# Performance work log

Measured on AMD Instinct MI355X. Metric: run time of the kernel, lower is better.

The kernel has to match this reference:

```python
import jax, jax.numpy as jnp
import numpy as np
from jax import lax

N, C_IN, C_OUT, H, W, K = 32, 512, 512, 56, 56, 7


def setup_inputs() -> dict:
    key = jax.random.key(0)
    ks = jax.random.split(key, 7)
    s_in = 1.0 / np.sqrt(C_IN)
    s_out = 1.0 / np.sqrt(C_OUT)
    return {
        "x": jax.random.normal(ks[0], (N, C_IN, H, W), dtype=jnp.float32),
        "k": K,
        "w_up": jax.random.normal(ks[1], (C_OUT, C_IN), dtype=jnp.float32) * s_in,
        "b_up": jax.random.normal(ks[2], (C_OUT,), dtype=jnp.float32) * s_in,
        "w_down": jax.random.normal(ks[3], (C_OUT, C_IN), dtype=jnp.float32) * s_in,
        "b_down": jax.random.normal(ks[4], (C_OUT,), dtype=jnp.float32) * s_in,
        "w_final": jax.random.normal(ks[5], (C_OUT, C_OUT), dtype=jnp.float32) * s_out,
        "b_final": jax.random.normal(ks[6], (C_OUT,), dtype=jnp.float32) * s_out,
    }


def _conv1x1(x, w, b):
    # x: [N, Cin, H, W], w: [Cout, Cin] -> [N, Cout, H, W]
    return jnp.einsum("nchw,oc->nohw", x, w) + b[None, :, None, None]


def reference(x, k, w_up, b_up, w_down, b_down, w_final, b_final):
    n, c_in, h, w = x.shape
    c_out = w_up.shape[0]
    pad = (k - 1) // 2

    up = _conv1x1(x, w_up, b_up)  # [N, Cout, H, W]

    # AdaptiveAvgPool2d(k): H, W divisible by k -> exact uniform pooling
    pooled = x.reshape(n, c_in, k, h // k, k, w // k).mean(axis=(3, 5))  # [N, Cin, k, k]
    down = _conv1x1(pooled, w_down, b_down)  # [N, Cout, k, k] dynamic depthwise kernels

    def dw_conv(u, ker):
        # u: [Cout, H, W], ker: [Cout, k, k]; depthwise (groups = Cout)
        return lax.conv_general_dilated(
            u[None],                    # [1, Cout, H, W]
            ker[:, None],               # [Cout, 1, k, k] (OIHW)
            window_strides=(1, 1),
            padding=[(pad, pad), (pad, pad)],
            feature_group_count=c_out,
            dimension_numbers=("NCHW", "OIHW", "NCHW"),
        )[0]

    out = jax.vmap(dw_conv)(up, down)  # [N, Cout, H, W]
    return _conv1x1(out, w_final, b_final)
```

## Files before the change

kernel.cpp:

```cpp
#include <hip/hip_runtime.h>
#include <hip/hip_bf16.h>

typedef unsigned short u16;
typedef _Float16 f16x8 __attribute__((ext_vector_type(8)));
typedef _Float16 f16x4 __attribute__((ext_vector_type(4)));
typedef _Float16 half2v __attribute__((ext_vector_type(2)));
typedef float f32x4 __attribute__((ext_vector_type(4)));
typedef unsigned short ushortx8 __attribute__((ext_vector_type(8)));
typedef unsigned short ushortx4 __attribute__((ext_vector_type(4)));

#define GPTR(p)  ((const __attribute__((address_space(1))) void*)(p))
#define LDSPTR(p) ((__attribute__((address_space(3))) void*)(p))

static __device__ __forceinline__ u16 f2h(float f) {
    _Float16 h = (_Float16)f;
    union { _Float16 h; u16 u; } v; v.h = h; return v.u;
}

__global__ __launch_bounds__(256) void cvtw_kernel(
    const float* __restrict__ wu, const float* __restrict__ wf,
    u16* __restrict__ wub, u16* __restrict__ wfb) {
    int i = blockIdx.x * 256 + threadIdx.x;
    wub[i] = f2h(wu[i]);
    wfb[i] = f2h(wf[i]);
}

__global__ __launch_bounds__(256) void transpose_kernel(
    const float* __restrict__ x, u16* __restrict__ xt) {
    __shared__ float tile[64][65];
    int bid = blockIdx.x;
    int jt = bid % 49;
    int r = bid / 49;
    int ct = r & 7, n = r >> 3;
    const float* src = x + ((size_t)(n * 512 + ct * 64)) * 3136 + jt * 64;
    for (int e = threadIdx.x; e < 4096; e += 256) {
        int i = e >> 6, jj = e & 63;
        tile[i][jj] = src[(size_t)i * 3136 + jj];
    }
    __syncthreads();
    u16* dst = xt + ((size_t)(n * 3136 + jt * 64)) * 512 + ct * 64;
    for (int e = threadIdx.x; e < 2048; e += 256) {
        int jj = e >> 5, i2 = (e & 31) * 2;
        unsigned int val = (unsigned)f2h(tile[i2][jj]) | ((unsigned)f2h(tile[i2 + 1][jj]) << 16);
        *(unsigned int*)(dst + (size_t)jj * 512 + i2) = val;
    }
}

__global__ __launch_bounds__(256) void poolh_kernel(
    const u16* __restrict__ xt, float* __restrict__ pooled) {
    int bid = blockIdx.x;
    int n = bid / 49, cell = bid - n * 49;
    int py = cell / 7, px = cell - py * 7;
    int t = threadIdx.x;
    float s0 = 0.f, s1 = 0.f;
    for (int r = 0; r < 8; ++r) {
        int h = py * 8 + r;
        const u16* base = xt + ((size_t)(n * 3136 + h * 56 + px * 8)) * 512 + 2 * t;
        #pragma unroll
        for (int cc = 0; cc < 8; ++cc) {
            half2v v = *(const half2v*)(base + (size_t)cc * 512);
            s0 += (float)v[0]; s1 += (float)v[1];
        }
    }
    float* pp = pooled + (size_t)n * 512 * 49 + py * 7 + px;
    pp[(size_t)(2 * t) * 49]     = s0 * (1.f / 64.f);
    pp[(size_t)(2 * t + 1) * 49] = s1 * (1.f / 64.f);
}

__global__ __launch_bounds__(256) void down_kernel(
    const float* __restrict__ pooled, const float* __restrict__ w_down,
    const float* __restrict__ b_down, float* __restrict__ down) {
    int bid = blockIdx.x;
    int n = bid >> 5, og = bid & 31;
    int wv = threadIdx.x >> 6, lane = threadIdx.x & 63;
    int o0 = og * 16 + wv * 4;
    const float* pp = pooled + (size_t)n * 512 * 49;
    const float* w0 = w_down + (size_t)o0 * 512;
    float a0 = 0, a1 = 0, a2 = 0, a3 = 0;
    int cell = lane < 49 ? lane : 48;
    #pragma unroll 4
    for (int c = 0; c < 512; ++c) {
        float p = pp[c * 49 + cell];
        a0 += p * w0[c];
        a1 += p * w0[512 + c];
        a2 += p * w0[1024 + c];
        a3 += p * w0[1536 + c];
    }
    if (lane < 49) {
        float* dd = down + ((size_t)n * 512 + o0) * 49 + lane;
        dd[0]   = a0 + b_down[o0];
        dd[49]  = a1 + b_down[o0 + 1];
        dd[98]  = a2 + b_down[o0 + 2];
        dd[147] = a3 + b_down[o0 + 3];
    }
}

template <int EPI>
__global__ __launch_bounds__(256) void gemm_kernel(
    const u16* __restrict__ A, const u16* __restrict__ Bt,
    const float* __restrict__ bias, void* __restrict__ Cout) {
    constexpr int K = 512;
    __shared__ u16 As[128 * 32];
    __shared__ u16 Bs[128 * 32];
    int tid = threadIdx.x, wv = tid >> 6, lane = tid & 63;
    int bid = blockIdx.x;
    int tm, tn;
    if (EPI == 0) { tm = (bid >> 5) * 8 + (bid & 7); tn = (bid >> 3) & 3; }
    else          { tn = (bid >> 5) * 8 + (bid & 7); tm = (bid >> 3) & 3; }
    size_t m0 = (size_t)tm * 128, n0 = (size_t)tn * 128;
    int lr = lane & 15, lk = (lane >> 4) * 8;
    int wr = wv >> 1, wc = wv & 1;

    int e0 = wv * 512 + lane * 8;
    int e1 = e0 + 2048;
    const u16* pa0 = A + (m0 + (size_t)(e0 >> 5)) * K + (e0 & 31);
    const u16* pa1 = A + (m0 + (size_t)(e1 >> 5)) * K + (e1 & 31);
    const u16* pb0 = Bt + (n0 + (size_t)(e0 >> 5)) * K + (e0 & 31);
    const u16* pb1 = Bt + (n0 + (size_t)(e1 >> 5)) * K + (e1 & 31);
    u16* sa0 = &As[wv * 512]; u16* sa1 = &As[wv * 512 + 2048];
    u16* sb0 = &Bs[wv * 512]; u16* sb1 = &Bs[wv * 512 + 2048];

    f32x4 acc[4][4] = {};

    for (int kt = 0; kt < K / 32; ++kt) {
        __builtin_amdgcn_global_load_lds(GPTR(pa0), LDSPTR(sa0), 16, 0, 0);
        __builtin_amdgcn_global_load_lds(GPTR(pa1), LDSPTR(sa1), 16, 0, 0);
        __builtin_amdgcn_global_load_lds(GPTR(pb0), LDSPTR(sb0), 16, 0, 0);
        __builtin_amdgcn_global_load_lds(GPTR(pb1), LDSPTR(sb1), 16, 0, 0);
        pa0 += 32; pa1 += 32; pb0 += 32; pb1 += 32;
        __syncthreads();
        f16x8 af[4], bfr[4];
        #pragma unroll
        for (int mi = 0; mi < 4; ++mi)
            af[mi] = *(const f16x8*)&As[(wr * 64 + mi * 16 + lr) * 32 + lk];
        #pragma unroll
        for (int ni = 0; ni < 4; ++ni)
            bfr[ni] = *(const f16x8*)&Bs[(wc * 64 + ni * 16 + lr) * 32 + lk];
        #pragma unroll
        for (int mi = 0; mi < 4; ++mi)
            #pragma unroll
            for (int ni = 0; ni < 4; ++ni)
                acc[mi][ni] = __builtin_amdgcn_mfma_f32_16x16x32_f16(af[mi], bfr[ni], acc[mi][ni], 0, 0, 0);
        __syncthreads();
    }

    if (EPI == 0) {
        u16* C = (u16*)Cout;
        #pragma unroll
        for (int ni = 0; ni < 4; ++ni) {
            size_t col = n0 + wc * 64 + ni * 16 + lr;
            float bv = bias[col];
            #pragma unroll
            for (int mi = 0; mi < 4; ++mi) {
                size_t rowb = m0 + wr * 64 + mi * 16 + (lane >> 4) * 4;
                ushortx4 pack;
                #pragma unroll
                for (int r = 0; r < 4; ++r)
                    pack[r] = f2h(acc[mi][ni][r] + bv);
                *(ushortx4*)&C[(rowb >> 3) * 4096 + col * 8 + (rowb & 7)] = pack;
            }
        }
    } else {
        float* C = (float*)Cout;
        #pragma unroll
        for (int ni = 0; ni < 4; ++ni) {
            int col = (int)(n0 + wc * 64 + ni * 16 + lr);
            int nimg = col / 3136;
            int jj = col - nimg * 3136;
            size_t obase = (size_t)nimg * 512 * 3136 + jj;
            #pragma unroll
            for (int mi = 0; mi < 4; ++mi) {
                int row = (int)(m0 + wr * 64 + mi * 16 + (lane >> 4) * 4);
                #pragma unroll
                for (int r = 0; r < 4; ++r)
                    C[obase + (size_t)(row + r) * 3136] = acc[mi][ni][r] + bias[row + r];
            }
        }
    }
}

__global__ __launch_bounds__(256) void dw_kernel(
    const u16* __restrict__ upb, const float* __restrict__ down,
    u16* __restrict__ dw) {
    __shared__ u16 tile[14 * 16 * 72];
    int bid = blockIdx.x;
    int n = bid / 224;
    int rem = bid - n * 224;
    int rt = rem >> 5;
    int cg = rem & 31;
    int tid = threadIdx.x;

    if (tid < 224)
        *(ushortx8*)&tile[tid * 72 + 56] = (ushortx8)0;

    for (int e = tid; e < 1568; e += 256) {
        int c = e & 15;
        int p = e >> 4;
        int hh = p / 7, jb = p - hh * 7;
        int h = rt * 8 + hh - 3;
        ushortx8 v = (ushortx8)0;
        if ((unsigned)h < 56u)
            v = *(const ushortx8*)(upb + ((size_t)(n * 392 + h * 7 + jb)) * 4096 + (cg * 16 + c) * 8);
        *(ushortx8*)&tile[(hh * 16 + c) * 72 + jb * 8] = v;
    }

    int c = tid & 15, u = tid >> 4;
    int row = u >> 1, wh = u & 1, w0 = wh * 28;
    const float* kp = down + ((size_t)n * 512 + cg * 16 + c) * 49;
    half2v kE[7][4], kO[7][4];
    #pragma unroll
    for (int ky = 0; ky < 7; ++ky) {
        float k0 = kp[ky*7+0], k1 = kp[ky*7+1], k2 = kp[ky*7+2], k3 = kp[ky*7+3];
        float k4 = kp[ky*7+4], k5 = kp[ky*7+5], k6 = kp[ky*7+6];
        kE[ky][0] = half2v{(_Float16)0.f, (_Float16)k0};
        kE[ky][1] = half2v{(_Float16)k1,  (_Float16)k2};
        kE[ky][2] = half2v{(_Float16)k3,  (_Float16)k4};
        kE[ky][3] = half2v{(_Float16)k5,  (_Float16)k6};
        kO[ky][0] = half2v{(_Float16)k0,  (_Float16)k1};
        kO[ky][1] = half2v{(_Float16)k2,  (_Float16)k3};
        kO[ky][2] = half2v{(_Float16)k4,  (_Float16)k5};
        kO[ky][3] = half2v{(_Float16)k6,  (_Float16)0.f};
    }
    __syncthreads();

    float acc[28];
    #pragma unroll
    for (int i = 0; i < 28; ++i) acc[i] = 0.f;

    #pragma unroll
    for (int ky = 0; ky < 7; ++ky) {
        const u16* rp = &tile[((row + ky) * 16 + c) * 72];
        half2v w2[18];
        #pragma unroll
        for (int t = 0; t < 9; ++t) {
            int p0 = ((w0 >> 1) - 2 + 2 * t) & 31;
            f16x4 q = *(const f16x4*)(rp + p0 * 2);
            w2[2*t]   = half2v{q[0], q[1]};
            w2[2*t+1] = half2v{q[2], q[3]};
        }
        #pragma unroll
        for (int m = 0; m < 14; ++m) {
            float ae = acc[2*m], ao = acc[2*m+1];
            ae = __builtin_amdgcn_fdot2(w2[m],   kE[ky][0], ae, false);
            ae = __builtin_amdgcn_fdot2(w2[m+1], kE[ky][1], ae, false);
            ae = __builtin_amdgcn_fdot2(w2[m+2], kE[ky][2], ae, false);
            ae = __builtin_amdgcn_fdot2(w2[m+3], kE[ky][3], ae, false);
            ao = __builtin_amdgcn_fdot2(w2[m+1], kO[ky][0], ao, false);
            ao = __builtin_amdgcn_fdot2(w2[m+2], kO[ky][1], ao, false);
            ao = __builtin_amdgcn_fdot2(w2[m+3], kO[ky][2], ao, false);
            ao = __builtin_amdgcn_fdot2(w2[m+4], kO[ky][3], ao, false);
            acc[2*m] = ae; acc[2*m+1] = ao;
        }
    }

    int h = rt * 8 + row;
    u16* op = dw + ((size_t)(n * 3136 + h * 56 + w0)) * 512 + cg * 16 + c;
    #pragma unroll
    for (int i = 0; i < 28; ++i)
        op[(size_t)i * 512] = f2h(acc[i]);
}

extern "C" void kernel_launch(void* const* d_in, const int* in_sizes, int n_in,
                              void* d_out, int out_size, void* d_ws, size_t ws_size,
                              hipStream_t stream) {
    const float* x       = (const float*)d_in[0];
    const float* w_up    = (const float*)d_in[2];
    const float* b_up    = (const float*)d_in[3];
    const float* w_down  = (const float*)d_in[4];
    const float* b_down  = (const float*)d_in[5];
    const float* w_final = (const float*)d_in[6];
    const float* b_final = (const float*)d_in[7];

    char* ws = (char*)d_ws;
    u16*   xt     = (u16*)  (ws + 0);
    u16*   upb    = (u16*)  (ws + 102760448);
    float* pooled = (float*)(ws + 205520896);
    float* down   = (float*)(ws + 208732160);
    u16*   wub    = (u16*)  (ws + 211943424);
    u16*   wfb    = (u16*)  (ws + 212467712);
    u16*   dwb    = xt;

    cvtw_kernel<<<1024, 256, 0, stream>>>(w_up, w_final, wub, wfb);
    transpose_kernel<<<12544, 256, 0, stream>>>(x, xt);
    poolh_kernel<<<1568, 256, 0, stream>>>(xt, pooled);
    down_kernel<<<1024, 256, 0, stream>>>(pooled, w_down, b_down, down);
    gemm_kernel<0><<<3136, 256, 0, stream>>>(xt, wub, b_up, upb);
    dw_kernel<<<7168, 256, 0, stream>>>(upb, down, dwb);
    gemm_kernel<1><<<3136, 256, 0, stream>>>(wfb, dwb, b_final, d_out);
}
```

Measured before the change: 410.6 us.

## Double-buffer GEMM LDS tiles and reorder depthwise block mapping

The GEMM main loop now uses two LDS buffers, prefetching the next K-slice via global_load_lds while MFMAs run on the current slice. This replaces two syncthreads per iteration with one waitcnt plus barrier, aiming to hide global load latency at the cost of doubled LDS (32KB per block), which may lower occupancy. The depthwise kernel's block index decomposition is also reordered so that consecutive blocks share a row tile across images and channel groups, changing L2 access locality.

```diff
diff --git a/kernel.cpp b/kernel.cpp
--- a/kernel.cpp
+++ b/kernel.cpp
@@ -100,8 +100,8 @@
     const u16* __restrict__ A, const u16* __restrict__ Bt,
     const float* __restrict__ bias, void* __restrict__ Cout) {
     constexpr int K = 512;
-    __shared__ u16 As[128 * 32];
-    __shared__ u16 Bs[128 * 32];
+    __shared__ u16 As[2][4096];
+    __shared__ u16 Bs[2][4096];
     int tid = threadIdx.x, wv = tid >> 6, lane = tid & 63;
     int bid = blockIdx.x;
     int tm, tn;
@@ -117,31 +117,44 @@
     const u16* pa1 = A + (m0 + (size_t)(e1 >> 5)) * K + (e1 & 31);
     const u16* pb0 = Bt + (n0 + (size_t)(e0 >> 5)) * K + (e0 & 31);
     const u16* pb1 = Bt + (n0 + (size_t)(e1 >> 5)) * K + (e1 & 31);
-    u16* sa0 = &As[wv * 512]; u16* sa1 = &As[wv * 512 + 2048];
-    u16* sb0 = &Bs[wv * 512]; u16* sb1 = &Bs[wv * 512 + 2048];
 
     f32x4 acc[4][4] = {};
 
+    {
+        __builtin_amdgcn_global_load_lds(GPTR(pa0), LDSPTR(&As[0][wv * 512]), 16, 0, 0);
+        __builtin_amdgcn_global_load_lds(GPTR(pa1), LDSPTR(&As[0][wv * 512 + 2048]), 16, 0, 0);
+        __builtin_amdgcn_global_load_lds(GPTR(pb0), LDSPTR(&Bs[0][wv * 512]), 16, 0, 0);
+        __builtin_amdgcn_global_load_lds(GPTR(pb1), LDSPTR(&Bs[0][wv * 512 + 2048]), 16, 0, 0);
+        pa0 += 32; pa1 += 32; pb0 += 32; pb1 += 32;
+    }
+    asm volatile("s_waitcnt vmcnt(0)" ::: "memory");
+    __builtin_amdgcn_s_barrier();
+
+    int cur = 0;
     for (int kt = 0; kt < K / 32; ++kt) {
-        __builtin_amdgcn_global_load_lds(GPTR(pa0), LDSPTR(sa0), 16, 0, 0);
-        __builtin_amdgcn_global_load_lds(GPTR(pa1), LDSPTR(sa1), 16, 0, 0);
-        __builtin_amdgcn_global_load_lds(GPTR(pb0), LDSPTR(sb0), 16, 0, 0);
-        __builtin_amdgcn_global_load_lds(GPTR(pb1), LDSPTR(sb1), 16, 0, 0);
-        pa0 += 32; pa1 += 32; pb0 += 32; pb1 += 32;
-        __syncthreads();
+        if (kt < K / 32 - 1) {
+            int nb = cur ^ 1;
+            __builtin_amdgcn_global_load_lds(GPTR(pa0), LDSPTR(&As[nb][wv * 512]), 16, 0, 0);
+            __builtin_amdgcn_global_load_lds(GPTR(pa1), LDSPTR(&As[nb][wv * 512 + 2048]), 16, 0, 0);
+            __builtin_amdgcn_global_load_lds(GPTR(pb0), LDSPTR(&Bs[nb][wv * 512]), 16, 0, 0);
+            __builtin_amdgcn_global_load_lds(GPTR(pb1), LDSPTR(&Bs[nb][wv * 512 + 2048]), 16, 0, 0);
+            pa0 += 32; pa1 += 32; pb0 += 32; pb1 += 32;
+        }
         f16x8 af[4], bfr[4];
         #pragma unroll
         for (int mi = 0; mi < 4; ++mi)
-            af[mi] = *(const f16x8*)&As[(wr * 64 + mi * 16 + lr) * 32 + lk];
+            af[mi] = *(const f16x8*)&As[cur][(wr * 64 + mi * 16 + lr) * 32 + lk];
         #pragma unroll
         for (int ni = 0; ni < 4; ++ni)
-            bfr[ni] = *(const f16x8*)&Bs[(wc * 64 + ni * 16 + lr) * 32 + lk];
+            bfr[ni] = *(const f16x8*)&Bs[cur][(wc * 64 + ni * 16 + lr) * 32 + lk];
         #pragma unroll
         for (int mi = 0; mi < 4; ++mi)
             #pragma unroll
             for (int ni = 0; ni < 4; ++ni)
                 acc[mi][ni] = __builtin_amdgcn_mfma_f32_16x16x32_f16(af[mi], bfr[ni], acc[mi][ni], 0, 0, 0);
-        __syncthreads();
+        asm volatile("s_waitcnt vmcnt(0)" ::: "memory");
+        __builtin_amdgcn_s_barrier();
+        cur ^= 1;
     }
 
     if (EPI == 0) {
@@ -184,10 +197,10 @@
     u16* __restrict__ dw) {
     __shared__ u16 tile[14 * 16 * 72];
     int bid = blockIdx.x;
-    int n = bid / 224;
-    int rem = bid - n * 224;
-    int rt = rem >> 5;
-    int cg = rem & 31;
+    int rt = bid >> 10;
+    int pair = bid & 1023;
+    int n = pair >> 5;
+    int cg = pair & 31;
     int tid = threadIdx.x;
 
     if (tid < 224)
```

Result: slower. 426.6 us (+3.9%).

## Triple-buffer GEMM LDS tiles with async prefetch two stages ahead

Applied to the files above, without the earlier changes.

Replaces the single-buffered load-sync-compute loop in the fp16 MFMA GEMM with a three-stage LDS ring. Global-to-LDS loads for tile kt+2 are issued before computing tile kt, and explicit vmcnt waits let earlier tiles finish while later ones are still in flight. The goal is to hide global memory latency behind MFMA work. In exchange it triples the LDS footprint, which may lower occupancy, and it depends on hand-counted vmcnt values being correct.

```diff
diff --git a/kernel.cpp b/kernel.cpp
--- a/kernel.cpp
+++ b/kernel.cpp
@@ -95,13 +95,21 @@
     }
 }
 
+#define STAGE(buf) do { \
+    __builtin_amdgcn_global_load_lds(GPTR(pa0), LDSPTR(&As[buf][wv * 512]), 16, 0, 0); \
+    __builtin_amdgcn_global_load_lds(GPTR(pa1), LDSPTR(&As[buf][wv * 512 + 2048]), 16, 0, 0); \
+    __builtin_amdgcn_global_load_lds(GPTR(pb0), LDSPTR(&Bs[buf][wv * 512]), 16, 0, 0); \
+    __builtin_amdgcn_global_load_lds(GPTR(pb1), LDSPTR(&Bs[buf][wv * 512 + 2048]), 16, 0, 0); \
+    pa0 += 32; pa1 += 32; pb0 += 32; pb1 += 32; } while (0)
+
 template <int EPI>
 __global__ __launch_bounds__(256) void gemm_kernel(
     const u16* __restrict__ A, const u16* __restrict__ Bt,
     const float* __restrict__ bias, void* __restrict__ Cout) {
     constexpr int K = 512;
-    __shared__ u16 As[128 * 32];
-    __shared__ u16 Bs[128 * 32];
+    constexpr int NT = K / 32;
+    __shared__ u16 As[3][4096];
+    __shared__ u16 Bs[3][4096];
     int tid = threadIdx.x, wv = tid >> 6, lane = tid & 63;
     int bid = blockIdx.x;
     int tm, tn;
@@ -117,31 +125,40 @@
     const u16* pa1 = A + (m0 + (size_t)(e1 >> 5)) * K + (e1 & 31);
     const u16* pb0 = Bt + (n0 + (size_t)(e0 >> 5)) * K + (e0 & 31);
     const u16* pb1 = Bt + (n0 + (size_t)(e1 >> 5)) * K + (e1 & 31);
-    u16* sa0 = &As[wv * 512]; u16* sa1 = &As[wv * 512 + 2048];
-    u16* sb0 = &Bs[wv * 512]; u16* sb1 = &Bs[wv * 512 + 2048];
 
     f32x4 acc[4][4] = {};
 
-    for (int kt = 0; kt < K / 32; ++kt) {
-        __builtin_amdgcn_global_load_lds(GPTR(pa0), LDSPTR(sa0), 16, 0, 0);
-        __builtin_amdgcn_global_load_lds(GPTR(pa1), LDSPTR(sa1), 16, 0, 0);
-        __builtin_amdgcn_global_load_lds(GPTR(pb0), LDSPTR(sb0), 16, 0, 0);
-        __builtin_amdgcn_global_load_lds(GPTR(pb1), LDSPTR(sb1), 16, 0, 0);
-        pa0 += 32; pa1 += 32; pb0 += 32; pb1 += 32;
-        __syncthreads();
+    STAGE(0);
+    STAGE(1);
+
+    int cur = 0, stg = 2;
+    for (int kt = 0; kt < NT; ++kt) {
+        if (kt + 2 < NT) {
+            STAGE(stg);
+            asm volatile("s_waitcnt vmcnt(8)" ::: "memory");
+        } else if (kt + 1 < NT) {
+            asm volatile("s_waitcnt vmcnt(4)" ::: "memory");
+        } else {
+            asm volatile("s_waitcnt vmcnt(0)" ::: "memory");
+        }
+        __builtin_amdgcn_s_barrier();
+
         f16x8 af[4], bfr[4];
         #pragma unroll
         for (int mi = 0; mi < 4; ++mi)
-            af[mi] = *(const f16x8*)&As[(wr * 64 + mi * 16 + lr) * 32 + lk];
+            af[mi] = *(const f16x8*)&As[cur][(wr * 64 + mi * 16 + lr) * 32 + lk];
         #pragma unroll
         for (int ni = 0; ni < 4; ++ni)
-            bfr[ni] = *(const f16x8*)&Bs[(wc * 64 + ni * 16 + lr) * 32 + lk];
+            bfr[ni] = *(const f16x8*)&Bs[cur][(wc * 64 + ni * 16 + lr) * 32 + lk];
         #pragma unroll
         for (int mi = 0; mi < 4; ++mi)
             #pragma unroll
             for (int ni = 0; ni < 4; ++ni)
                 acc[mi][ni] = __builtin_amdgcn_mfma_f32_16x16x32_f16(af[mi], bfr[ni], acc[mi][ni], 0, 0, 0);
-        __syncthreads();
+
+        __builtin_amdgcn_s_barrier();
+        cur = (cur == 2) ? 0 : cur + 1;
+        stg = (stg == 2) ? 0 : stg + 1;
     }
 
     if (EPI == 0) {
```

Measured after the change: 413.8 us. No clear change (+0.8%).

## Rewrite 1x1-conv GEMMs as 8-wave 128x256 tiles with multi-stage LDS pipeline

Applied to the files above, without the earlier changes.

Both GEMM launches now use a 512-thread kernel that computes 128x256 output tiles instead of 128x128. Operand tiles are prefetched into multi-buffered LDS (up to four stages) with global_load_lds, and the LDS layout uses an XOR swizzle. Split barriers and s_setprio interleave the prefetch issue with MFMA blocks. The aim is to hide global-load latency, avoid the two full __syncthreads per k-step, and cut LDS bank conflicts and per-tile operand traffic. In exchange it uses more LDS per block, which may limit occupancy, and depends on hand-tuned vmcnt waits being correct.

```diff
diff --git a/kernel.cpp b/kernel.cpp
--- a/kernel.cpp
+++ b/kernel.cpp
@@ -95,53 +95,88 @@
     }
 }
 
+#define STAGE_M(bufi, kt) do { \
+    __builtin_amdgcn_global_load_lds(GPTR(srcM + (size_t)(kt) * 32), LDSPTR(&Mb[bufi][wv * 512]), 16, 0, 0); \
+  } while (0)
+#define STAGE_N(bufi, kt) do { \
+    __builtin_amdgcn_global_load_lds(GPTR(srcN + (size_t)(kt) * 32), LDSPTR(&Nb[bufi][wv * 512]), 16, 0, 0); \
+    __builtin_amdgcn_global_load_lds(GPTR(srcN + 65536 + (size_t)(kt) * 32), LDSPTR(&Nb[bufi][4096 + wv * 512]), 16, 0, 0); \
+  } while (0)
+
 template <int EPI>
-__global__ __launch_bounds__(256) void gemm_kernel(
+__global__ __launch_bounds__(512, 4) void gemm8_kernel(
     const u16* __restrict__ A, const u16* __restrict__ Bt,
     const float* __restrict__ bias, void* __restrict__ Cout) {
-    constexpr int K = 512;
-    __shared__ u16 As[128 * 32];
-    __shared__ u16 Bs[128 * 32];
-    int tid = threadIdx.x, wv = tid >> 6, lane = tid & 63;
+    constexpr int NT = 16;
+    constexpr int DM = EPI ? 2 : 4;
+    constexpr int DN = EPI ? 4 : 2;
+    constexpr int SLoads = EPI ? 1 : 2;
+    __shared__ u16 Mb[DM][4096];
+    __shared__ u16 Nb[DN][8192];
+
+    int tid = threadIdx.x;
+    int wv = tid >> 6, l = tid & 63;
+    int lr = l & 15, lk = (l >> 4) * 8;
+    int wr = wv & 1, wc = wv >> 1;
     int bid = blockIdx.x;
     int tm, tn;
-    if (EPI == 0) { tm = (bid >> 5) * 8 + (bid & 7); tn = (bid >> 3) & 3; }
+    if (EPI == 0) { tm = (bid >> 4) * 8 + (bid & 7); tn = (bid >> 3) & 1; }
     else          { tn = (bid >> 5) * 8 + (bid & 7); tm = (bid >> 3) & 3; }
-    size_t m0 = (size_t)tm * 128, n0 = (size_t)tn * 128;
-    int lr = lane & 15, lk = (lane >> 4) * 8;
-    int wr = wv >> 1, wc = wv & 1;
-
-    int e0 = wv * 512 + lane * 8;
-    int e1 = e0 + 2048;
-    const u16* pa0 = A + (m0 + (size_t)(e0 >> 5)) * K + (e0 & 31);
-    const u16* pa1 = A + (m0 + (size_t)(e1 >> 5)) * K + (e1 & 31);
-    const u16* pb0 = Bt + (n0 + (size_t)(e0 >> 5)) * K + (e0 & 31);
-    const u16* pb1 = Bt + (n0 + (size_t)(e1 >> 5)) * K + (e1 & 31);
-    u16* sa0 = &As[wv * 512]; u16* sa1 = &As[wv * 512 + 2048];
-    u16* sb0 = &Bs[wv * 512]; u16* sb1 = &Bs[wv * 512 + 2048];
+    size_t m0 = (size_t)tm * 128, n0 = (size_t)tn * 256;
+
+    int r = tid >> 2;
+    int kx = ((tid & 3) * 8) ^ (((r >> 1) & 3) << 3);
+    const u16* srcM = A  + (m0 + (size_t)r) * 512 + kx;
+    const u16* srcN = Bt + (n0 + (size_t)r) * 512 + kx;
+    int aswz = ((lr >> 1) & 3) << 3;
+
+    if (EPI == 0) { STAGE_M(0, 0); STAGE_M(1, 1); STAGE_M(2, 2); STAGE_N(0, 0); STAGE_N(1, 1); }
+    else          { STAGE_N(0, 0); STAGE_N(1, 1); STAGE_N(2, 2); STAGE_M(0, 0); STAGE_M(1, 1); }
+    asm volatile("s_waitcnt vmcnt(%0)" :: "n"(SLoads) : "memory");
+    __builtin_amdgcn_s_barrier();
 
     f32x4 acc[4][4] = {};
 
-    for (int kt = 0; kt < K / 32; ++kt) {
-        __builtin_amdgcn_global_load_lds(GPTR(pa0), LDSPTR(sa0), 16, 0, 0);
-        __builtin_amdgcn_global_load_lds(GPTR(pa1), LDSPTR(sa1), 16, 0, 0);
-        __builtin_amdgcn_global_load_lds(GPTR(pb0), LDSPTR(sb0), 16, 0, 0);
-        __builtin_amdgcn_global_load_lds(GPTR(pb1), LDSPTR(sb1), 16, 0, 0);
-        pa0 += 32; pa1 += 32; pb0 += 32; pb1 += 32;
-        __syncthreads();
-        f16x8 af[4], bfr[4];
-        #pragma unroll
-        for (int mi = 0; mi < 4; ++mi)
-            af[mi] = *(const f16x8*)&As[(wr * 64 + mi * 16 + lr) * 32 + lk];
+    for (int j = 0; j < NT; ++j) {
+        int mb = EPI ? (j & 1) : (j & 3);
+        int nb = EPI ? (j & 3) : (j & 1);
+        f16x8 af0 = *(const f16x8*)&Mb[mb][(wr * 64 +  0 + lr) * 32 + (lk ^ aswz)];
+        f16x8 af1 = *(const f16x8*)&Mb[mb][(wr * 64 + 16 + lr) * 32 + (lk ^ aswz)];
+        f16x8 af2 = *(const f16x8*)&Mb[mb][(wr * 64 + 32 + lr) * 32 + (lk ^ aswz)];
+        f16x8 af3 = *(const f16x8*)&Mb[mb][(wr * 64 + 48 + lr) * 32 + (lk ^ aswz)];
+        f16x8 bfr[4];
         #pragma unroll
         for (int ni = 0; ni < 4; ++ni)
-            bfr[ni] = *(const f16x8*)&Bs[(wc * 64 + ni * 16 + lr) * 32 + lk];
-        #pragma unroll
-        for (int mi = 0; mi < 4; ++mi)
-            #pragma unroll
-            for (int ni = 0; ni < 4; ++ni)
-                acc[mi][ni] = __builtin_amdgcn_mfma_f32_16x16x32_f16(af[mi], bfr[ni], acc[mi][ni], 0, 0, 0);
-        __syncthreads();
+            bfr[ni] = *(const f16x8*)&Nb[nb][(wc * 64 + ni * 16 + lr) * 32 + (lk ^ aswz)];
+        if (j + 3 < NT) {
+            if (EPI == 0) STAGE_M((j + 3) & 3, j + 3);
+            else          STAGE_N((j + 3) & 3, j + 3);
+        }
+        __builtin_amdgcn_s_barrier();
+        __builtin_amdgcn_s_setprio(1);
+        #pragma unroll
+        for (int ni = 0; ni < 4; ++ni) {
+            acc[0][ni] = __builtin_amdgcn_mfma_f32_16x16x32_f16(af0, bfr[ni], acc[0][ni], 0, 0, 0);
+            acc[1][ni] = __builtin_amdgcn_mfma_f32_16x16x32_f16(af1, bfr[ni], acc[1][ni], 0, 0, 0);
+        }
+        __builtin_amdgcn_s_setprio(0);
+        __builtin_amdgcn_s_barrier();
+        if (j + 2 < NT) {
+            if (EPI == 0) STAGE_N((j + 2) & 1, j + 2);
+            else          STAGE_M((j + 2) & 1, j + 2);
+        }
+        __builtin_amdgcn_s_barrier();
+        __builtin_amdgcn_s_setprio(1);
+        #pragma unroll
+        for (int ni = 0; ni < 4; ++ni) {
+            acc[2][ni] = __builtin_amdgcn_mfma_f32_16x16x32_f16(af2, bfr[ni], acc[2][ni], 0, 0, 0);
+            acc[3][ni] = __builtin_amdgcn_mfma_f32_16x16x32_f16(af3, bfr[ni], acc[3][ni], 0, 0, 0);
+        }
+        __builtin_amdgcn_s_setprio(0);
+        if (j <= NT - 4)       asm volatile("s_waitcnt vmcnt(3)" ::: "memory");
+        else if (j == NT - 3)  asm volatile("s_waitcnt vmcnt(%0)" :: "n"(SLoads) : "memory");
+        else                   asm volatile("s_waitcnt vmcnt(0)" ::: "memory");
+        __builtin_amdgcn_s_barrier();
     }
 
     if (EPI == 0) {
@@ -152,11 +187,11 @@
             float bv = bias[col];
             #pragma unroll
             for (int mi = 0; mi < 4; ++mi) {
-                size_t rowb = m0 + wr * 64 + mi * 16 + (lane >> 4) * 4;
+                size_t rowb = m0 + wr * 64 + mi * 16 + (l >> 4) * 4;
                 ushortx4 pack;
                 #pragma unroll
-                for (int r = 0; r < 4; ++r)
-                    pack[r] = f2h(acc[mi][ni][r] + bv);
+                for (int rr = 0; rr < 4; ++rr)
+                    pack[rr] = f2h(acc[mi][ni][rr] + bv);
                 *(ushortx4*)&C[(rowb >> 3) * 4096 + col * 8 + (rowb & 7)] = pack;
             }
         }
@@ -170,10 +205,10 @@
             size_t obase = (size_t)nimg * 512 * 3136 + jj;
             #pragma unroll
             for (int mi = 0; mi < 4; ++mi) {
-                int row = (int)(m0 + wr * 64 + mi * 16 + (lane >> 4) * 4);
+                int row = (int)(m0 + wr * 64 + mi * 16 + (l >> 4) * 4);
                 #pragma unroll
-                for (int r = 0; r < 4; ++r)
-                    C[obase + (size_t)(row + r) * 3136] = acc[mi][ni][r] + bias[row + r];
+                for (int rr = 0; rr < 4; ++rr)
+                    C[obase + (size_t)(row + rr) * 3136] = acc[mi][ni][rr] + bias[row + rr];
             }
         }
     }
@@ -284,7 +319,7 @@
     transpose_kernel<<<12544, 256, 0, stream>>>(x, xt);
     poolh_kernel<<<1568, 256, 0, stream>>>(xt, pooled);
     down_kernel<<<1024, 256, 0, stream>>>(pooled, w_down, b_down, down);
-    gemm_kernel<0><<<3136, 256, 0, stream>>>(xt, wub, b_up, upb);
+    gemm8_kernel<0><<<1568, 512, 0, stream>>>(xt, wub, b_up, upb);
     dw_kernel<<<7168, 256, 0, stream>>>(upb, down, dwb);
-    gemm_kernel<1><<<3136, 256, 0, stream>>>(wfb, dwb, b_final, d_out);
-}
+    gemm8_kernel<1><<<1568, 512, 0, stream>>>(wfb, dwb, b_final, d_out);
+}
```

Result: no change. 412.6 us (+0.5%).
